# Performance work log

Hardware: AMD Instinct MI355X
Metric: run time of the kernel (lower is better)

Reference implementation:

```python
import jax, jax.numpy as jnp
import numpy as np
import math

S, N, L = 4, 10000, 8
IN, H = 64, 64
D = IN + 2 * H + 1  # rnn input: feats + bidirectional walk enc + degree


def _gru(x, h0, Wih, Whh, bih, bhh, reverse=False):
    """Torch-semantics GRU. x: (B, L, Din), h0: (B, H). Gate order r,z,n."""
    xw = jnp.einsum('bld,gd->blg', x, Wih) + bih  # precompute input proj (B,L,3H)

    def step(h, xw_t):
        gh = h @ Whh.T + bhh
        xr, xz, xn = jnp.split(xw_t, 3, axis=-1)
        hr, hz, hn = jnp.split(gh, 3, axis=-1)
        r = jax.nn.sigmoid(xr + hr)
        z = jax.nn.sigmoid(xz + hz)
        n = jnp.tanh(xn + r * hn)
        h = (1.0 - z) * n + z * h
        return h, h

    hT, ys = jax.lax.scan(step, h0, jnp.swapaxes(xw, 0, 1), reverse=reverse)
    return jnp.swapaxes(ys, 0, 1), hT  # (B,L,H), (B,H)


def setup_inputs() -> dict:
    key = jax.random.key(0)
    ks = jax.random.split(key, 16)
    w = lambda k, shape: (jax.random.normal(k, shape, jnp.float32) * 0.1)
    inp = {
        'h': jax.random.normal(ks[0], (N, IN), jnp.float32),
        'walks': jax.random.randint(ks[1], (S, N, L), 0, N, dtype=jnp.int32),
        'in_degrees': jax.random.randint(ks[2], (N,), 1, 50, dtype=jnp.int32),
        # bidirectional walk GRU (input=2)
        'Wih_f': w(ks[3], (3 * H, 2)), 'Whh_f': w(ks[4], (3 * H, H)),
        'bih_f': w(ks[5], (3 * H,)), 'bhh_f': w(ks[6], (3 * H,)),
        'Wih_b': w(ks[7], (3 * H, 2)), 'Whh_b': w(ks[8], (3 * H, H)),
        'bih_b': w(ks[9], (3 * H,)), 'bhh_b': w(ks[10], (3 * H,)),
        # main GRU (input=D)
        'Wih': w(ks[11], (3 * H, D)), 'Whh': w(ks[12], (3 * H, H)),
        'bih': w(ks[13], (3 * H,)), 'bhh': w(ks[14], (3 * H,)),
    }
    return inp


def reference(h, walks, in_degrees, Wih_f, Whh_f, bih_f, bhh_f,
              Wih_b, Whh_b, bih_b, bhh_b, Wih, Whh, bih, bhh):
    S_, N_, L_ = walks.shape
    # uniqueness: first-occurrence index of each node within its walk
    eq = walks[..., :, None] == walks[..., None, :]          # (S,N,L,L)
    u = jnp.argmax(eq, axis=-1).astype(h.dtype)              # (S,N,L)
    walks = walks[..., ::-1]
    u = u[..., ::-1]
    u = (u / L_) * (2.0 * math.pi)
    uw = jnp.stack([jnp.sin(u), jnp.cos(u)], axis=-1)        # (S,N,L,2)

    hw = h[walks]                                            # gather (S,N,L,IN)
    deg = in_degrees.astype(h.dtype)[walks][..., None]       # (S,N,L,1)
    deg = deg / deg.max()

    B = S_ * N_
    uw2 = uw.reshape(B, L_, 2)
    h0 = jnp.zeros((B, H), h.dtype)
    yf, hf = _gru(uw2, h0, Wih_f, Whh_f, bih_f, bhh_f)
    yb, hb = _gru(uw2, h0, Wih_b, Whh_b, bih_b, bhh_b, reverse=True)
    y_walk = jnp.concatenate([yf, yb], axis=-1).reshape(S_, N_, L_, 2 * H)
    h_walk = 0.5 * (hf + hb)                                 # mean over directions (B,H)

    x = jnp.concatenate([hw, y_walk, deg], axis=-1).reshape(B, L_, D)
    _, hT = _gru(x, h_walk, Wih, Whh, bih, bhh)
    # final hidden has layer dim of size 1; .mean(0) is identity -> (S,N,H)
    out = hT.reshape(S_, N_, H)
    return out
```

## Files before the change

### kernel.cpp

```cpp
#include <hip/hip_runtime.h>
#include <hip/hip_bf16.h>

#define NN   10000
#define SS   4
#define BB   40000
#define LLEN 8
#define DD   193
#define G3   192

typedef __attribute__((ext_vector_type(8))) short bf16x8;
typedef __attribute__((ext_vector_type(4))) short short4v;
typedef __attribute__((ext_vector_type(4))) float f32x4;

#define OFF_DMAX 0
#define OFF_DEGN 1024
#define OFF_A    65536
#define OFF_YF   (8ull*1024*1024)
#define OFF_YB   (49ull*1024*1024)
#define OFF_HFB  (90ull*1024*1024)

__device__ __forceinline__ float sigm(float x){ return 1.0f/(1.0f+__expf(-x)); }
__device__ __forceinline__ float tanh_(float x){
  float e = __expf(-2.0f*fabsf(x));
  float t = (1.0f-e)/(1.0f+e);
  return x>=0.0f ? t : -t;
}
__device__ __forceinline__ short f2b(float f){
  unsigned u = __builtin_bit_cast(unsigned, f);
  u = u + 0x7FFFu + ((u>>16)&1u);
  return (short)(u>>16);
}
__device__ __forceinline__ float b2f(short s){
  unsigned u = ((unsigned)(unsigned short)s)<<16;
  return __builtin_bit_cast(float, u);
}

__global__ void k_zero(int* dmax){
  if (threadIdx.x==0 && blockIdx.x==0) *dmax = 0;
}

__global__ void k_degmax(const int* __restrict__ walks, const int* __restrict__ indeg,
                         int* __restrict__ dmax){
  int i = blockIdx.x*blockDim.x + threadIdx.x;
  int d = 0;
  if (i < SS*NN*LLEN) d = indeg[walks[i]];
  #pragma unroll
  for (int off=32; off>0; off>>=1) d = max(d, __shfl_xor(d, off));
  if ((threadIdx.x&63)==0 && d>0) atomicMax(dmax, d);
}

__global__ void k_degn(const int* __restrict__ indeg, const int* __restrict__ dmax,
                       float* __restrict__ degn){
  int n = blockIdx.x*blockDim.x + threadIdx.x;
  if (n < NN) degn[n] = (float)indeg[n] / (float)(*dmax);
}

__global__ __launch_bounds__(192) void k_A(const float* __restrict__ h,
                                           const float* __restrict__ Wih,
                                           const float* __restrict__ bih,
                                           float* __restrict__ A){
  int g = threadIdx.x;
  float w[64];
  #pragma unroll
  for (int k=0;k<64;++k) w[k] = Wih[g*DD + k];
  float bg = bih[g];
  __shared__ float hs[64];
  int n0 = blockIdx.x*32;
  for (int j=0;j<32;++j){
    int n = n0 + j;
    if (n >= NN) break;
    __syncthreads();
    if (g < 64) hs[g] = h[n*64+g];
    __syncthreads();
    float acc = bg;
    #pragma unroll
    for (int k=0;k<64;++k) acc += w[k]*hs[k];
    A[n*G3 + g] = acc;
  }
}

__global__ __launch_bounds__(256,3) void k_fb(
    const int* __restrict__ walks,
    const float* __restrict__ Wih_f, const float* __restrict__ Whh_f,
    const float* __restrict__ bih_f, const float* __restrict__ bhh_f,
    const float* __restrict__ Wih_b, const float* __restrict__ Whh_b,
    const float* __restrict__ bih_b, const float* __restrict__ bhh_b,
    short* __restrict__ yf_out, short* __restrict__ yb_out,
    short* __restrict__ hfb)
{
  const int dir = blockIdx.y;
  const float* Wih = dir ? Wih_b : Wih_f;
  const float* Whh = dir ? Whh_b : Whh_f;
  const float* bih = dir ? bih_b : bih_f;
  const float* bhh = dir ? bhh_b : bhh_f;
  short* yout = dir ? yb_out : yf_out;

  __shared__ __align__(16) short Wlds[192*64];
  __shared__ __align__(16) short A2[192*8];
  __shared__ __align__(16) short hl[64*64];
  __shared__ __align__(16) float sc[64*8*2];
  __shared__ __align__(16) float bhn[64];

  const int tid = threadIdx.x;
  const int b0  = blockIdx.x*64;

  for (int idx = tid; idx < 192*64; idx += 256){
    int g = idx>>6, k = idx&63;
    Wlds[g*64 + (k ^ ((g&7)<<3))] = f2b(Whh[idx]);
  }
  for (int g = tid; g < 192; g += 256){
    A2[g*8+0] = f2b(Wih[2*g]);
    A2[g*8+1] = f2b(Wih[2*g+1]);
    float bb = bih[g] + (g < 128 ? bhh[g] : 0.0f);
    A2[g*8+2] = f2b(bb);
    A2[g*8+3]=0; A2[g*8+4]=0; A2[g*8+5]=0; A2[g*8+6]=0; A2[g*8+7]=0;
  }
  if (tid < 64) bhn[tid] = bhh[128+tid];
  for (int idx = tid; idx < 512; idx += 256){
    int s = idx>>3, t = idx&7, p = 7-t;
    const int* wr = walks + (long)(b0+s)*LLEN;
    int wp = wr[p]; int u = 7;
    #pragma unroll
    for (int j=7;j>=0;--j) if (wr[j]==wp) u = j;
    float si, ci;
    __sincosf((float)u * 0.7853981633974483f, &si, &ci);
    sc[idx*2] = si; sc[idx*2+1] = ci;
  }
  __syncthreads();

  const int lane = tid & 63;
  const int wv   = tid >> 6;
  const int c    = lane & 15;
  const int a    = lane >> 4;
  const int s    = wv*16 + c;
  const int sg   = b0 + s;

  float hreg[4][4];
  short4v z4 = {0,0,0,0};
  #pragma unroll
  for (int q=0;q<4;++q){
    #pragma unroll
    for (int r=0;r<4;++r) hreg[q][r] = 0.0f;
    int i0 = q*16 + 4*a;
    *(short4v*)&hl[s*64 + (i0 ^ ((s&7)<<3))] = z4;
  }

  for (int ss=0; ss<8; ++ss){
    const int t = dir ? 7-ss : ss;
    asm volatile("s_waitcnt lgkmcnt(0)" ::: "memory");
    bf16x8 bh0 = *(const bf16x8*)&hl[s*64 + ((a*8)      ^ ((s&7)<<3))];
    bf16x8 bh1 = *(const bf16x8*)&hl[s*64 + ((32 + a*8) ^ ((s&7)<<3))];
    bf16x8 b2 = {0,0,0,0,0,0,0,0};
    if (a == 0){
      b2[0] = f2b(sc[(s*8+t)*2]);
      b2[1] = f2b(sc[(s*8+t)*2+1]);
      b2[2] = (short)0x3F80;
    }
    f32x4 acc1[12]; f32x4 acc2[4];
    #pragma unroll
    for (int T=0;T<12;++T){ acc1[T].x=0;acc1[T].y=0;acc1[T].z=0;acc1[T].w=0; }
    #pragma unroll
    for (int T=0;T<4;++T){ acc2[T].x=0;acc2[T].y=0;acc2[T].z=0;acc2[T].w=0; }

    #pragma unroll
    for (int T=0;T<12;++T){
      int g = 16*T + c;
      bf16x8 a0 = *(const bf16x8*)&Wlds[g*64 + ((a*8)      ^ ((g&7)<<3))];
      bf16x8 a1 = *(const bf16x8*)&Wlds[g*64 + ((32 + a*8) ^ ((g&7)<<3))];
      acc1[T] = __builtin_amdgcn_mfma_f32_16x16x32_bf16(a0, bh0, acc1[T], 0,0,0);
      acc1[T] = __builtin_amdgcn_mfma_f32_16x16x32_bf16(a1, bh1, acc1[T], 0,0,0);
      bf16x8 a2 = *(const bf16x8*)&A2[g*8];
      if (T < 8) acc1[T]   = __builtin_amdgcn_mfma_f32_16x16x32_bf16(a2, b2, acc1[T],   0,0,0);
      else       acc2[T-8] = __builtin_amdgcn_mfma_f32_16x16x32_bf16(a2, b2, acc2[T-8], 0,0,0);
    }

    #pragma unroll
    for (int q=0;q<4;++q){
      int i0 = q*16 + 4*a;
      f32x4 bv = *(const f32x4*)&bhn[i0];
      short4v pack;
      #pragma unroll
      for (int r=0;r<4;++r){
        float rr = sigm(acc1[q][r]);
        float zz = sigm(acc1[4+q][r]);
        float hn = acc1[8+q][r] + bv[r];
        float xn = acc2[q][r];
        float nn = tanh_(xn + rr*hn);
        float hv = (1.0f-zz)*nn + zz*hreg[q][r];
        hreg[q][r] = hv;
        pack[r] = f2b(hv);
      }
      *(short4v*)&hl[s*64 + (i0 ^ ((s&7)<<3))] = pack;
      int kb = 4*q + a;
      *(short4v*)(yout + ((long)(t*16+kb)*BB + sg)*4) = pack;
    }
  }

  #pragma unroll
  for (int q=0;q<4;++q){
    int i0 = q*16 + 4*a;
    short4v pk;
    #pragma unroll
    for (int r=0;r<4;++r) pk[r] = f2b(hreg[q][r]);
    *(short4v*)(hfb + ((long)dir*BB + sg)*64 + i0) = pk;
  }
}

__global__ __launch_bounds__(256,1) void k_final(
    const int* __restrict__ walks, const float* __restrict__ degn,
    const float* __restrict__ A,
    const float* __restrict__ W, const float* __restrict__ U,
    const float* __restrict__ bhh,
    const short* __restrict__ yf, const short* __restrict__ yb,
    const short* __restrict__ hfb,
    float* __restrict__ out)
{
  __shared__ __align__(16) short Ulds[192*64];
  __shared__ __align__(16) short Wy[192*128];
  __shared__ __align__(16) short A5[192*8];
  __shared__ __align__(16) short hl[64*64];
  __shared__ __align__(16) int   node[64*8];
  __shared__ __align__(16) float degl[64*8];
  __shared__ __align__(16) float bhn[64];

  const int tid = threadIdx.x;
  const int b0  = blockIdx.x*64;

  for (int idx = tid; idx < 192*64; idx += 256){
    int g = idx>>6, k = idx&63;
    Ulds[g*64 + (k ^ ((g&7)<<3))] = f2b(U[idx]);
  }
  for (int idx = tid; idx < 192*128; idx += 256){
    int g = idx>>7, k2 = idx&127;
    Wy[g*128 + (k2 ^ ((g&7)<<3))] = f2b(W[(long)g*DD + 64 + k2]);
  }
  for (int g = tid; g < 192; g += 256){
    A5[g*8+0] = f2b(W[(long)g*DD + 192]);
    A5[g*8+1] = (g < 128) ? f2b(bhh[g]) : (short)0;
    A5[g*8+2]=0; A5[g*8+3]=0; A5[g*8+4]=0; A5[g*8+5]=0; A5[g*8+6]=0; A5[g*8+7]=0;
  }
  if (tid < 64) bhn[tid] = bhh[128+tid];
  for (int idx = tid; idx < 512; idx += 256){
    int s = idx>>3, t = idx&7;
    int nd = walks[(long)(b0+s)*LLEN + 7-t];
    node[idx] = nd;
    degl[idx] = degn[nd];
  }
  __syncthreads();

  const int lane = tid & 63;
  const int wv   = tid >> 6;
  const int c    = lane & 15;
  const int a    = lane >> 4;
  const int s    = wv*16 + c;
  const int sg   = b0 + s;

  float hreg[4][4];
  #pragma unroll
  for (int q=0;q<4;++q){
    int i0 = q*16 + 4*a;
    short4v hf4 = *(const short4v*)(hfb + (long)sg*64 + i0);
    short4v hb4 = *(const short4v*)(hfb + ((long)BB + sg)*64 + i0);
    short4v pk;
    #pragma unroll
    for (int r=0;r<4;++r){
      float hv = 0.5f*(b2f(hf4[r]) + b2f(hb4[r]));
      hreg[q][r] = hv;
      pk[r] = f2b(hv);
    }
    *(short4v*)&hl[s*64 + (i0 ^ ((s&7)<<3))] = pk;
  }

  auto ldy = [&](const short* Y, int t, int kh, bf16x8& dst){
    int ky0 = kh*32 + a*8;
    int kb  = ky0 >> 2;
    long base = ((long)(t*16 + kb)*BB + sg)*4;
    short4v lo = *(const short4v*)(Y + base);
    short4v hi = *(const short4v*)(Y + base + (long)BB*4);
    dst[0]=lo[0]; dst[1]=lo[1]; dst[2]=lo[2]; dst[3]=lo[3];
    dst[4]=hi[0]; dst[5]=hi[1]; dst[6]=hi[2]; dst[7]=hi[3];
  };

  bf16x8 yfc[2], ybc[2];
  ldy(yf, 0, 0, yfc[0]); ldy(yf, 0, 1, yfc[1]);
  ldy(yb, 0, 0, ybc[0]); ldy(yb, 0, 1, ybc[1]);

  for (int t=0; t<8; ++t){
    bf16x8 yfn[2], ybn[2];
    if (t < 7){
      ldy(yf, t+1, 0, yfn[0]); ldy(yf, t+1, 1, yfn[1]);
      ldy(yb, t+1, 0, ybn[0]); ldy(yb, t+1, 1, ybn[1]);
    }
    int nd = node[s*8 + t];
    f32x4 Ag[12];
    #pragma unroll
    for (int T=0;T<12;++T) Ag[T] = *(const f32x4*)(A + (long)nd*192 + 16*T + 4*a);

    asm volatile("s_waitcnt lgkmcnt(0)" ::: "memory");
    bf16x8 bh0 = *(const bf16x8*)&hl[s*64 + ((a*8)      ^ ((s&7)<<3))];
    bf16x8 bh1 = *(const bf16x8*)&hl[s*64 + ((32 + a*8) ^ ((s&7)<<3))];
    bf16x8 b5 = {0,0,0,0,0,0,0,0};
    if (a == 0){
      b5[0] = f2b(degl[s*8+t]);
      b5[1] = (short)0x3F80;
    }

    f32x4 acc1[12]; f32x4 acc2[4];
    #pragma unroll
    for (int T=0;T<12;++T){ acc1[T].x=0;acc1[T].y=0;acc1[T].z=0;acc1[T].w=0; }
    #pragma unroll
    for (int T=0;T<4;++T){ acc2[T].x=0;acc2[T].y=0;acc2[T].z=0;acc2[T].w=0; }

    #pragma unroll
    for (int T=0;T<12;++T){
      int g = 16*T + c;
      bf16x8 u0 = *(const bf16x8*)&Ulds[g*64 + ((a*8)      ^ ((g&7)<<3))];
      bf16x8 u1 = *(const bf16x8*)&Ulds[g*64 + ((32 + a*8) ^ ((g&7)<<3))];
      acc1[T] = __builtin_amdgcn_mfma_f32_16x16x32_bf16(u0, bh0, acc1[T], 0,0,0);
      acc1[T] = __builtin_amdgcn_mfma_f32_16x16x32_bf16(u1, bh1, acc1[T], 0,0,0);
      bf16x8 w0 = *(const bf16x8*)&Wy[g*128 + ((a*8)       ^ ((g&7)<<3))];
      bf16x8 w1 = *(const bf16x8*)&Wy[g*128 + ((32 + a*8)  ^ ((g&7)<<3))];
      bf16x8 w2 = *(const bf16x8*)&Wy[g*128 + ((64 + a*8)  ^ ((g&7)<<3))];
      bf16x8 w3 = *(const bf16x8*)&Wy[g*128 + ((96 + a*8)  ^ ((g&7)<<3))];
      bf16x8 a5 = *(const bf16x8*)&A5[g*8];
      if (T < 8){
        acc1[T] = __builtin_amdgcn_mfma_f32_16x16x32_bf16(w0, yfc[0], acc1[T], 0,0,0);
        acc1[T] = __builtin_amdgcn_mfma_f32_16x16x32_bf16(w1, yfc[1], acc1[T], 0,0,0);
        acc1[T] = __builtin_amdgcn_mfma_f32_16x16x32_bf16(w2, ybc[0], acc1[T], 0,0,0);
        acc1[T] = __builtin_amdgcn_mfma_f32_16x16x32_bf16(w3, ybc[1], acc1[T], 0,0,0);
        acc1[T] = __builtin_amdgcn_mfma_f32_16x16x32_bf16(a5, b5,     acc1[T], 0,0,0);
      } else {
        acc2[T-8] = __builtin_amdgcn_mfma_f32_16x16x32_bf16(w0, yfc[0], acc2[T-8], 0,0,0);
        acc2[T-8] = __builtin_amdgcn_mfma_f32_16x16x32_bf16(w1, yfc[1], acc2[T-8], 0,0,0);
        acc2[T-8] = __builtin_amdgcn_mfma_f32_16x16x32_bf16(w2, ybc[0], acc2[T-8], 0,0,0);
        acc2[T-8] = __builtin_amdgcn_mfma_f32_16x16x32_bf16(w3, ybc[1], acc2[T-8], 0,0,0);
        acc2[T-8] = __builtin_amdgcn_mfma_f32_16x16x32_bf16(a5, b5,     acc2[T-8], 0,0,0);
      }
    }

    #pragma unroll
    for (int q=0;q<4;++q){
      int i0 = q*16 + 4*a;
      f32x4 bv = *(const f32x4*)&bhn[i0];
      short4v pack;
      #pragma unroll
      for (int r=0;r<4;++r){
        float rr = sigm(acc1[q][r]   + Ag[q][r]);
        float zz = sigm(acc1[4+q][r] + Ag[4+q][r]);
        float hn = acc1[8+q][r] + bv[r];
        float xn = acc2[q][r]   + Ag[8+q][r];
        float nn = tanh_(xn + rr*hn);
        float hv = (1.0f-zz)*nn + zz*hreg[q][r];
        hreg[q][r] = hv;
        pack[r] = f2b(hv);
      }
      *(short4v*)&hl[s*64 + (i0 ^ ((s&7)<<3))] = pack;
    }

    if (t < 7){
      yfc[0]=yfn[0]; yfc[1]=yfn[1];
      ybc[0]=ybn[0]; ybc[1]=ybn[1];
    }
  }

  #pragma unroll
  for (int q=0;q<4;++q){
    int i0 = q*16 + 4*a;
    f32x4 o;
    #pragma unroll
    for (int r=0;r<4;++r) o[r] = hreg[q][r];
    *(f32x4*)(out + (long)sg*64 + i0) = o;
  }
}

extern "C" void kernel_launch(void* const* d_in, const int* in_sizes, int n_in,
                              void* d_out, int out_size, void* d_ws, size_t ws_size,
                              hipStream_t stream) {
  const float* h     = (const float*)d_in[0];
  const int*   walks = (const int*)d_in[1];
  const int*   indeg = (const int*)d_in[2];
  const float* Wf    = (const float*)d_in[3];
  const float* Uf    = (const float*)d_in[4];
  const float* bif   = (const float*)d_in[5];
  const float* bhf   = (const float*)d_in[6];
  const float* Wb    = (const float*)d_in[7];
  const float* Ub    = (const float*)d_in[8];
  const float* bib   = (const float*)d_in[9];
  const float* bhb   = (const float*)d_in[10];
  const float* W     = (const float*)d_in[11];
  const float* U     = (const float*)d_in[12];
  const float* bi    = (const float*)d_in[13];
  const float* bh    = (const float*)d_in[14];
  float* out = (float*)d_out;

  char* ws = (char*)d_ws;
  int*   dmax = (int*)(ws + OFF_DMAX);
  float* degn = (float*)(ws + OFF_DEGN);
  float* A    = (float*)(ws + OFF_A);
  short* yfw  = (short*)(ws + OFF_YF);
  short* ybw  = (short*)(ws + OFF_YB);
  short* hfb  = (short*)(ws + OFF_HFB);

  k_zero<<<1, 64, 0, stream>>>(dmax);
  k_degmax<<<(SS*NN*LLEN + 255)/256, 256, 0, stream>>>(walks, indeg, dmax);
  k_degn<<<(NN + 255)/256, 256, 0, stream>>>(indeg, dmax, degn);
  k_A<<<(NN + 31)/32, 192, 0, stream>>>(h, W, bi, A);
  k_fb<<<dim3(BB/64, 2), 256, 0, stream>>>(walks,
                                           Wf, Uf, bif, bhf,
                                           Wb, Ub, bib, bhb,
                                           yfw, ybw, hfb);
  k_final<<<BB/64, 256, 0, stream>>>(walks, degn, A, W, U, bh,
                                     yfw, ybw, hfb, out);
}
```

Before: 383.5 us.

## Prepack weights into MFMA fragment blob and drop per-block LDS weight staging

A new prep kernel converts all GRU weights and bias vectors once into bf16, laid out in MFMA A-fragment order in global memory. k_fb and k_final then read these fragments straight from global/L2 instead of having every block convert and stage the full weight matrices in LDS. Blocks shrink to 128 threads, each wave now handles two 16-sequence groups so every weight fragment load feeds two MFMAs, and LDS use drops so more blocks fit per CU. The cost is repeated weight fragment loads from cache on every timestep. The prefetch of y inputs for the next step in k_final is also removed.

```diff
diff --git a/kernel.cpp b/kernel.cpp
--- a/kernel.cpp
+++ b/kernel.cpp
@@ -14,10 +14,14 @@
 
 #define OFF_DMAX 0
 #define OFF_DEGN 1024
-#define OFF_A    65536
+#define OFF_FRAG 65536
+#define OFF_A    262144
 #define OFF_YF   (8ull*1024*1024)
 #define OFF_YB   (49ull*1024*1024)
 #define OFF_HFB  (90ull*1024*1024)
+
+#define FB_FRAG(dir,T,ch)  (((dir)*12 + (T))*3 + (ch))
+#define FIN_FRAG(T,ch)     (72 + (T)*7 + (ch))
 
 __device__ __forceinline__ float sigm(float x){ return 1.0f/(1.0f+__expf(-x)); }
 __device__ __forceinline__ float tanh_(float x){
@@ -53,6 +57,58 @@
                        float* __restrict__ degn){
   int n = blockIdx.x*blockDim.x + threadIdx.x;
   if (n < NN) degn[n] = (float)indeg[n] / (float)(*dmax);
+}
+
+__global__ __launch_bounds__(64) void k_prep(
+    const float* __restrict__ Wih_f, const float* __restrict__ Whh_f,
+    const float* __restrict__ bih_f, const float* __restrict__ bhh_f,
+    const float* __restrict__ Wih_b, const float* __restrict__ Whh_b,
+    const float* __restrict__ bih_b, const float* __restrict__ bhh_b,
+    const float* __restrict__ W, const float* __restrict__ U,
+    const float* __restrict__ bhh,
+    short* __restrict__ blob)
+{
+  int f = blockIdx.x;
+  int lane = threadIdx.x;
+  int c = lane & 15, a = lane >> 4;
+  float v[8];
+  if (f < 72){
+    int dir = f / 36, rem = f % 36, T = rem / 3, ch = rem % 3;
+    int g = 16*T + c;
+    const float* Whh = dir ? Whh_b : Whh_f;
+    const float* Wih = dir ? Wih_b : Wih_f;
+    const float* bih = dir ? bih_b : bih_f;
+    const float* bhd = dir ? bhh_b : bhh_f;
+    if (ch < 2){
+      #pragma unroll
+      for (int j=0;j<8;++j) v[j] = Whh[g*64 + ch*32 + a*8 + j];
+    } else {
+      #pragma unroll
+      for (int j=0;j<8;++j){
+        int k = a*8 + j;
+        v[j] = (k==0) ? Wih[2*g] : (k==1) ? Wih[2*g+1]
+             : (k==2) ? (bih[g] + (g<128 ? bhd[g] : 0.0f)) : 0.0f;
+      }
+    }
+  } else {
+    int f2 = f - 72, T = f2 / 7, ch = f2 % 7;
+    int g = 16*T + c;
+    if (ch < 2){
+      #pragma unroll
+      for (int j=0;j<8;++j) v[j] = U[g*64 + ch*32 + a*8 + j];
+    } else if (ch < 6){
+      #pragma unroll
+      for (int j=0;j<8;++j) v[j] = W[(long)g*DD + 64 + (ch-2)*32 + a*8 + j];
+    } else {
+      #pragma unroll
+      for (int j=0;j<8;++j){
+        int k = a*8 + j;
+        v[j] = (k==0) ? W[(long)g*DD + 192] : (k==1) ? (g<128 ? bhh[g] : 0.0f) : 0.0f;
+      }
+    }
+  }
+  #pragma unroll
+  for (int j=0;j<8;++j) blob[(long)f*512 + lane*8 + j] = f2b(v[j]);
 }
 
 __global__ __launch_bounds__(192) void k_A(const float* __restrict__ h,
@@ -79,24 +135,16 @@
   }
 }
 
-__global__ __launch_bounds__(256,3) void k_fb(
-    const int* __restrict__ walks,
-    const float* __restrict__ Wih_f, const float* __restrict__ Whh_f,
-    const float* __restrict__ bih_f, const float* __restrict__ bhh_f,
-    const float* __restrict__ Wih_b, const float* __restrict__ Whh_b,
-    const float* __restrict__ bih_b, const float* __restrict__ bhh_b,
+__global__ __launch_bounds__(128, 2) void k_fb(
+    const int* __restrict__ walks, const short* __restrict__ blob,
+    const float* __restrict__ bhh_f, const float* __restrict__ bhh_b,
     short* __restrict__ yf_out, short* __restrict__ yb_out,
     short* __restrict__ hfb)
 {
   const int dir = blockIdx.y;
-  const float* Wih = dir ? Wih_b : Wih_f;
-  const float* Whh = dir ? Whh_b : Whh_f;
-  const float* bih = dir ? bih_b : bih_f;
   const float* bhh = dir ? bhh_b : bhh_f;
   short* yout = dir ? yb_out : yf_out;
 
-  __shared__ __align__(16) short Wlds[192*64];
-  __shared__ __align__(16) short A2[192*8];
   __shared__ __align__(16) short hl[64*64];
   __shared__ __align__(16) float sc[64*8*2];
   __shared__ __align__(16) float bhn[64];
@@ -104,19 +152,8 @@
   const int tid = threadIdx.x;
   const int b0  = blockIdx.x*64;
 
-  for (int idx = tid; idx < 192*64; idx += 256){
-    int g = idx>>6, k = idx&63;
-    Wlds[g*64 + (k ^ ((g&7)<<3))] = f2b(Whh[idx]);
-  }
-  for (int g = tid; g < 192; g += 256){
-    A2[g*8+0] = f2b(Wih[2*g]);
-    A2[g*8+1] = f2b(Wih[2*g+1]);
-    float bb = bih[g] + (g < 128 ? bhh[g] : 0.0f);
-    A2[g*8+2] = f2b(bb);
-    A2[g*8+3]=0; A2[g*8+4]=0; A2[g*8+5]=0; A2[g*8+6]=0; A2[g*8+7]=0;
-  }
   if (tid < 64) bhn[tid] = bhh[128+tid];
-  for (int idx = tid; idx < 512; idx += 256){
+  for (int idx = tid; idx < 512; idx += 128){
     int s = idx>>3, t = idx&7, p = 7-t;
     const int* wr = walks + (long)(b0+s)*LLEN;
     int wp = wr[p]; int u = 7;
@@ -126,98 +163,115 @@
     __sincosf((float)u * 0.7853981633974483f, &si, &ci);
     sc[idx*2] = si; sc[idx*2+1] = ci;
   }
-  __syncthreads();
 
   const int lane = tid & 63;
   const int wv   = tid >> 6;
   const int c    = lane & 15;
   const int a    = lane >> 4;
-  const int s    = wv*16 + c;
-  const int sg   = b0 + s;
-
-  float hreg[4][4];
+  const int s0   = wv*32 + c;
+  const int s1   = wv*32 + 16 + c;
+
+  float hreg[2][4][4];
   short4v z4 = {0,0,0,0};
   #pragma unroll
-  for (int q=0;q<4;++q){
-    #pragma unroll
-    for (int r=0;r<4;++r) hreg[q][r] = 0.0f;
-    int i0 = q*16 + 4*a;
-    *(short4v*)&hl[s*64 + (i0 ^ ((s&7)<<3))] = z4;
-  }
+  for (int sb=0;sb<2;++sb){
+    int s = sb ? s1 : s0;
+    #pragma unroll
+    for (int q=0;q<4;++q){
+      #pragma unroll
+      for (int r=0;r<4;++r) hreg[sb][q][r] = 0.0f;
+      int i0 = q*16 + 4*a;
+      *(short4v*)&hl[s*64 + (i0 ^ ((s&7)<<3))] = z4;
+    }
+  }
+  __syncthreads();
+
+  const bf16x8* FB = (const bf16x8*)blob;
 
   for (int ss=0; ss<8; ++ss){
     const int t = dir ? 7-ss : ss;
     asm volatile("s_waitcnt lgkmcnt(0)" ::: "memory");
-    bf16x8 bh0 = *(const bf16x8*)&hl[s*64 + ((a*8)      ^ ((s&7)<<3))];
-    bf16x8 bh1 = *(const bf16x8*)&hl[s*64 + ((32 + a*8) ^ ((s&7)<<3))];
-    bf16x8 b2 = {0,0,0,0,0,0,0,0};
-    if (a == 0){
-      b2[0] = f2b(sc[(s*8+t)*2]);
-      b2[1] = f2b(sc[(s*8+t)*2+1]);
-      b2[2] = (short)0x3F80;
-    }
-    f32x4 acc1[12]; f32x4 acc2[4];
-    #pragma unroll
-    for (int T=0;T<12;++T){ acc1[T].x=0;acc1[T].y=0;acc1[T].z=0;acc1[T].w=0; }
-    #pragma unroll
-    for (int T=0;T<4;++T){ acc2[T].x=0;acc2[T].y=0;acc2[T].z=0;acc2[T].w=0; }
-
-    #pragma unroll
-    for (int T=0;T<12;++T){
-      int g = 16*T + c;
-      bf16x8 a0 = *(const bf16x8*)&Wlds[g*64 + ((a*8)      ^ ((g&7)<<3))];
-      bf16x8 a1 = *(const bf16x8*)&Wlds[g*64 + ((32 + a*8) ^ ((g&7)<<3))];
-      acc1[T] = __builtin_amdgcn_mfma_f32_16x16x32_bf16(a0, bh0, acc1[T], 0,0,0);
-      acc1[T] = __builtin_amdgcn_mfma_f32_16x16x32_bf16(a1, bh1, acc1[T], 0,0,0);
-      bf16x8 a2 = *(const bf16x8*)&A2[g*8];
-      if (T < 8) acc1[T]   = __builtin_amdgcn_mfma_f32_16x16x32_bf16(a2, b2, acc1[T],   0,0,0);
-      else       acc2[T-8] = __builtin_amdgcn_mfma_f32_16x16x32_bf16(a2, b2, acc2[T-8], 0,0,0);
-    }
-
+    bf16x8 bh0[2], bh1[2], b2[2];
+    #pragma unroll
+    for (int sb=0;sb<2;++sb){
+      int s = sb ? s1 : s0;
+      bh0[sb] = *(const bf16x8*)&hl[s*64 + ((a*8)      ^ ((s&7)<<3))];
+      bh1[sb] = *(const bf16x8*)&hl[s*64 + ((32 + a*8) ^ ((s&7)<<3))];
+      float si = sc[(s*8+t)*2], ci = sc[(s*8+t)*2+1];
+      bf16x8 bb = {0,0,0,0,0,0,0,0};
+      if (a == 0){ bb[0] = f2b(si); bb[1] = f2b(ci); bb[2] = (short)0x3F80; }
+      b2[sb] = bb;
+    }
+
+    #pragma unroll
+    for (int q=0;q<4;++q){
+      f32x4 ar[2], az[2], an1[2], an2[2];
+      #pragma unroll
+      for (int sb=0;sb<2;++sb){
+        ar[sb].x=0;ar[sb].y=0;ar[sb].z=0;ar[sb].w=0;
+        az[sb]=ar[sb]; an1[sb]=ar[sb]; an2[sb]=ar[sb];
+      }
+      #pragma unroll
+      for (int ch=0;ch<3;++ch){
+        bf16x8 fr = FB[(long)FB_FRAG(dir,   q,ch)*64 + lane];
+        bf16x8 fz = FB[(long)FB_FRAG(dir, 4+q,ch)*64 + lane];
+        bf16x8 fn = FB[(long)FB_FRAG(dir, 8+q,ch)*64 + lane];
+        #pragma unroll
+        for (int sb=0;sb<2;++sb){
+          bf16x8 bb = (ch==0) ? bh0[sb] : (ch==1) ? bh1[sb] : b2[sb];
+          ar[sb] = __builtin_amdgcn_mfma_f32_16x16x32_bf16(fr, bb, ar[sb], 0,0,0);
+          az[sb] = __builtin_amdgcn_mfma_f32_16x16x32_bf16(fz, bb, az[sb], 0,0,0);
+          if (ch < 2) an1[sb] = __builtin_amdgcn_mfma_f32_16x16x32_bf16(fn, bb, an1[sb], 0,0,0);
+          else        an2[sb] = __builtin_amdgcn_mfma_f32_16x16x32_bf16(fn, bb, an2[sb], 0,0,0);
+        }
+      }
+      f32x4 bv = *(const f32x4*)&bhn[q*16 + 4*a];
+      #pragma unroll
+      for (int sb=0;sb<2;++sb){
+        int s = sb ? s1 : s0;
+        int sg = b0 + s;
+        short4v pack;
+        #pragma unroll
+        for (int r=0;r<4;++r){
+          float rr = sigm(ar[sb][r]);
+          float zz = sigm(az[sb][r]);
+          float hn_ = an1[sb][r] + bv[r];
+          float xn  = an2[sb][r];
+          float nn = tanh_(xn + rr*hn_);
+          float hv = (1.0f-zz)*nn + zz*hreg[sb][q][r];
+          hreg[sb][q][r] = hv;
+          pack[r] = f2b(hv);
+        }
+        int i0 = q*16 + 4*a;
+        *(short4v*)&hl[s*64 + (i0 ^ ((s&7)<<3))] = pack;
+        *(short4v*)(yout + ((long)(t*16 + 4*q + a)*BB + sg)*4) = pack;
+      }
+    }
+  }
+
+  #pragma unroll
+  for (int sb=0;sb<2;++sb){
+    int s = sb ? s1 : s0;
+    int sg = b0 + s;
     #pragma unroll
     for (int q=0;q<4;++q){
       int i0 = q*16 + 4*a;
-      f32x4 bv = *(const f32x4*)&bhn[i0];
-      short4v pack;
-      #pragma unroll
-      for (int r=0;r<4;++r){
-        float rr = sigm(acc1[q][r]);
-        float zz = sigm(acc1[4+q][r]);
-        float hn = acc1[8+q][r] + bv[r];
-        float xn = acc2[q][r];
-        float nn = tanh_(xn + rr*hn);
-        float hv = (1.0f-zz)*nn + zz*hreg[q][r];
-        hreg[q][r] = hv;
-        pack[r] = f2b(hv);
-      }
-      *(short4v*)&hl[s*64 + (i0 ^ ((s&7)<<3))] = pack;
-      int kb = 4*q + a;
-      *(short4v*)(yout + ((long)(t*16+kb)*BB + sg)*4) = pack;
-    }
-  }
-
-  #pragma unroll
-  for (int q=0;q<4;++q){
-    int i0 = q*16 + 4*a;
-    short4v pk;
-    #pragma unroll
-    for (int r=0;r<4;++r) pk[r] = f2b(hreg[q][r]);
-    *(short4v*)(hfb + ((long)dir*BB + sg)*64 + i0) = pk;
-  }
-}
-
-__global__ __launch_bounds__(256,1) void k_final(
+      short4v pk;
+      #pragma unroll
+      for (int r=0;r<4;++r) pk[r] = f2b(hreg[sb][q][r]);
+      *(short4v*)(hfb + ((long)dir*BB + sg)*64 + i0) = pk;
+    }
+  }
+}
+
+__global__ __launch_bounds__(128, 2) void k_final(
     const int* __restrict__ walks, const float* __restrict__ degn,
-    const float* __restrict__ A,
-    const float* __restrict__ W, const float* __restrict__ U,
+    const float* __restrict__ A, const short* __restrict__ blob,
     const float* __restrict__ bhh,
     const short* __restrict__ yf, const short* __restrict__ yb,
     const short* __restrict__ hfb,
     float* __restrict__ out)
 {
-  __shared__ __align__(16) short Ulds[192*64];
-  __shared__ __align__(16) short Wy[192*128];
-  __shared__ __align__(16) short A5[192*8];
   __shared__ __align__(16) short hl[64*64];
   __shared__ __align__(16) int   node[64*8];
   __shared__ __align__(16) float degl[64*8];
@@ -226,54 +280,47 @@
   const int tid = threadIdx.x;
   const int b0  = blockIdx.x*64;
 
-  for (int idx = tid; idx < 192*64; idx += 256){
-    int g = idx>>6, k = idx&63;
-    Ulds[g*64 + (k ^ ((g&7)<<3))] = f2b(U[idx]);
-  }
-  for (int idx = tid; idx < 192*128; idx += 256){
-    int g = idx>>7, k2 = idx&127;
-    Wy[g*128 + (k2 ^ ((g&7)<<3))] = f2b(W[(long)g*DD + 64 + k2]);
-  }
-  for (int g = tid; g < 192; g += 256){
-    A5[g*8+0] = f2b(W[(long)g*DD + 192]);
-    A5[g*8+1] = (g < 128) ? f2b(bhh[g]) : (short)0;
-    A5[g*8+2]=0; A5[g*8+3]=0; A5[g*8+4]=0; A5[g*8+5]=0; A5[g*8+6]=0; A5[g*8+7]=0;
-  }
   if (tid < 64) bhn[tid] = bhh[128+tid];
-  for (int idx = tid; idx < 512; idx += 256){
+  for (int idx = tid; idx < 512; idx += 128){
     int s = idx>>3, t = idx&7;
     int nd = walks[(long)(b0+s)*LLEN + 7-t];
     node[idx] = nd;
     degl[idx] = degn[nd];
   }
-  __syncthreads();
 
   const int lane = tid & 63;
   const int wv   = tid >> 6;
   const int c    = lane & 15;
   const int a    = lane >> 4;
-  const int s    = wv*16 + c;
-  const int sg   = b0 + s;
-
-  float hreg[4][4];
-  #pragma unroll
-  for (int q=0;q<4;++q){
-    int i0 = q*16 + 4*a;
-    short4v hf4 = *(const short4v*)(hfb + (long)sg*64 + i0);
-    short4v hb4 = *(const short4v*)(hfb + ((long)BB + sg)*64 + i0);
-    short4v pk;
-    #pragma unroll
-    for (int r=0;r<4;++r){
-      float hv = 0.5f*(b2f(hf4[r]) + b2f(hb4[r]));
-      hreg[q][r] = hv;
-      pk[r] = f2b(hv);
-    }
-    *(short4v*)&hl[s*64 + (i0 ^ ((s&7)<<3))] = pk;
-  }
-
-  auto ldy = [&](const short* Y, int t, int kh, bf16x8& dst){
-    int ky0 = kh*32 + a*8;
-    int kb  = ky0 >> 2;
+  const int s0   = wv*32 + c;
+  const int s1   = wv*32 + 16 + c;
+
+  float hreg[2][4][4];
+  #pragma unroll
+  for (int sb=0;sb<2;++sb){
+    int s = sb ? s1 : s0;
+    int sg = b0 + s;
+    #pragma unroll
+    for (int q=0;q<4;++q){
+      int i0 = q*16 + 4*a;
+      short4v hf4 = *(const short4v*)(hfb + (long)sg*64 + i0);
+      short4v hb4 = *(const short4v*)(hfb + ((long)BB + sg)*64 + i0);
+      short4v pk;
+      #pragma unroll
+      for (int r=0;r<4;++r){
+        float hv = 0.5f*(b2f(hf4[r]) + b2f(hb4[r]));
+        hreg[sb][q][r] = hv;
+        pk[r] = f2b(hv);
+      }
+      *(short4v*)&hl[s*64 + (i0 ^ ((s&7)<<3))] = pk;
+    }
+  }
+  __syncthreads();
+
+  const bf16x8* FB = (const bf16x8*)blob;
+
+  auto ldy = [&](const short* Y, int t, int kh, int sg, bf16x8& dst){
+    int kb  = kh*8 + a*2;
     long base = ((long)(t*16 + kb)*BB + sg)*4;
     short4v lo = *(const short4v*)(Y + base);
     short4v hi = *(const short4v*)(Y + base + (long)BB*4);
@@ -281,95 +328,86 @@
     dst[4]=hi[0]; dst[5]=hi[1]; dst[6]=hi[2]; dst[7]=hi[3];
   };
 
-  bf16x8 yfc[2], ybc[2];
-  ldy(yf, 0, 0, yfc[0]); ldy(yf, 0, 1, yfc[1]);
-  ldy(yb, 0, 0, ybc[0]); ldy(yb, 0, 1, ybc[1]);
-
   for (int t=0; t<8; ++t){
-    bf16x8 yfn[2], ybn[2];
-    if (t < 7){
-      ldy(yf, t+1, 0, yfn[0]); ldy(yf, t+1, 1, yfn[1]);
-      ldy(yb, t+1, 0, ybn[0]); ldy(yb, t+1, 1, ybn[1]);
-    }
-    int nd = node[s*8 + t];
-    f32x4 Ag[12];
-    #pragma unroll
-    for (int T=0;T<12;++T) Ag[T] = *(const f32x4*)(A + (long)nd*192 + 16*T + 4*a);
-
     asm volatile("s_waitcnt lgkmcnt(0)" ::: "memory");
-    bf16x8 bh0 = *(const bf16x8*)&hl[s*64 + ((a*8)      ^ ((s&7)<<3))];
-    bf16x8 bh1 = *(const bf16x8*)&hl[s*64 + ((32 + a*8) ^ ((s&7)<<3))];
-    bf16x8 b5 = {0,0,0,0,0,0,0,0};
-    if (a == 0){
-      b5[0] = f2b(degl[s*8+t]);
-      b5[1] = (short)0x3F80;
-    }
-
-    f32x4 acc1[12]; f32x4 acc2[4];
-    #pragma unroll
-    for (int T=0;T<12;++T){ acc1[T].x=0;acc1[T].y=0;acc1[T].z=0;acc1[T].w=0; }
-    #pragma unroll
-    for (int T=0;T<4;++T){ acc2[T].x=0;acc2[T].y=0;acc2[T].z=0;acc2[T].w=0; }
-
-    #pragma unroll
-    for (int T=0;T<12;++T){
-      int g = 16*T + c;
-      bf16x8 u0 = *(const bf16x8*)&Ulds[g*64 + ((a*8)      ^ ((g&7)<<3))];
-      bf16x8 u1 = *(const bf16x8*)&Ulds[g*64 + ((32 + a*8) ^ ((g&7)<<3))];
-      acc1[T] = __builtin_amdgcn_mfma_f32_16x16x32_bf16(u0, bh0, acc1[T], 0,0,0);
-      acc1[T] = __builtin_amdgcn_mfma_f32_16x16x32_bf16(u1, bh1, acc1[T], 0,0,0);
-      bf16x8 w0 = *(const bf16x8*)&Wy[g*128 + ((a*8)       ^ ((g&7)<<3))];
-      bf16x8 w1 = *(const bf16x8*)&Wy[g*128 + ((32 + a*8)  ^ ((g&7)<<3))];
-      bf16x8 w2 = *(const bf16x8*)&Wy[g*128 + ((64 + a*8)  ^ ((g&7)<<3))];
-      bf16x8 w3 = *(const bf16x8*)&Wy[g*128 + ((96 + a*8)  ^ ((g&7)<<3))];
-      bf16x8 a5 = *(const bf16x8*)&A5[g*8];
-      if (T < 8){
-        acc1[T] = __builtin_amdgcn_mfma_f32_16x16x32_bf16(w0, yfc[0], acc1[T], 0,0,0);
-        acc1[T] = __builtin_amdgcn_mfma_f32_16x16x32_bf16(w1, yfc[1], acc1[T], 0,0,0);
-        acc1[T] = __builtin_amdgcn_mfma_f32_16x16x32_bf16(w2, ybc[0], acc1[T], 0,0,0);
-        acc1[T] = __builtin_amdgcn_mfma_f32_16x16x32_bf16(w3, ybc[1], acc1[T], 0,0,0);
-        acc1[T] = __builtin_amdgcn_mfma_f32_16x16x32_bf16(a5, b5,     acc1[T], 0,0,0);
-      } else {
-        acc2[T-8] = __builtin_amdgcn_mfma_f32_16x16x32_bf16(w0, yfc[0], acc2[T-8], 0,0,0);
-        acc2[T-8] = __builtin_amdgcn_mfma_f32_16x16x32_bf16(w1, yfc[1], acc2[T-8], 0,0,0);
-        acc2[T-8] = __builtin_amdgcn_mfma_f32_16x16x32_bf16(w2, ybc[0], acc2[T-8], 0,0,0);
-        acc2[T-8] = __builtin_amdgcn_mfma_f32_16x16x32_bf16(w3, ybc[1], acc2[T-8], 0,0,0);
-        acc2[T-8] = __builtin_amdgcn_mfma_f32_16x16x32_bf16(a5, b5,     acc2[T-8], 0,0,0);
-      }
-    }
-
+    bf16x8 bh0[2], bh1[2], b5[2], yfc[2][2], ybc[2][2];
+    int nd_[2];
+    #pragma unroll
+    for (int sb=0;sb<2;++sb){
+      int s = sb ? s1 : s0;
+      int sg = b0 + s;
+      bh0[sb] = *(const bf16x8*)&hl[s*64 + ((a*8)      ^ ((s&7)<<3))];
+      bh1[sb] = *(const bf16x8*)&hl[s*64 + ((32 + a*8) ^ ((s&7)<<3))];
+      bf16x8 bb = {0,0,0,0,0,0,0,0};
+      if (a == 0){ bb[0] = f2b(degl[s*8+t]); bb[1] = (short)0x3F80; }
+      b5[sb] = bb;
+      ldy(yf, t, 0, sg, yfc[sb][0]); ldy(yf, t, 1, sg, yfc[sb][1]);
+      ldy(yb, t, 0, sg, ybc[sb][0]); ldy(yb, t, 1, sg, ybc[sb][1]);
+      nd_[sb] = node[s*8 + t];
+    }
+
+    #pragma unroll
+    for (int q=0;q<4;++q){
+      f32x4 ar[2], az[2], an1[2], an2[2];
+      #pragma unroll
+      for (int sb=0;sb<2;++sb){
+        ar[sb].x=0;ar[sb].y=0;ar[sb].z=0;ar[sb].w=0;
+        az[sb]=ar[sb]; an1[sb]=ar[sb]; an2[sb]=ar[sb];
+      }
+      #pragma unroll
+      for (int ch=0;ch<7;++ch){
+        bf16x8 fr = FB[(long)FIN_FRAG(   q,ch)*64 + lane];
+        bf16x8 fz = FB[(long)FIN_FRAG( 4+q,ch)*64 + lane];
+        bf16x8 fn = FB[(long)FIN_FRAG( 8+q,ch)*64 + lane];
+        #pragma unroll
+        for (int sb=0;sb<2;++sb){
+          bf16x8 bb = (ch==0) ? bh0[sb] : (ch==1) ? bh1[sb]
+                    : (ch==2) ? yfc[sb][0] : (ch==3) ? yfc[sb][1]
+                    : (ch==4) ? ybc[sb][0] : (ch==5) ? ybc[sb][1] : b5[sb];
+          ar[sb] = __builtin_amdgcn_mfma_f32_16x16x32_bf16(fr, bb, ar[sb], 0,0,0);
+          az[sb] = __builtin_amdgcn_mfma_f32_16x16x32_bf16(fz, bb, az[sb], 0,0,0);
+          if (ch < 2) an1[sb] = __builtin_amdgcn_mfma_f32_16x16x32_bf16(fn, bb, an1[sb], 0,0,0);
+          else        an2[sb] = __builtin_amdgcn_mfma_f32_16x16x32_bf16(fn, bb, an2[sb], 0,0,0);
+        }
+      }
+      f32x4 bv = *(const f32x4*)&bhn[q*16 + 4*a];
+      #pragma unroll
+      for (int sb=0;sb<2;++sb){
+        int s = sb ? s1 : s0;
+        const float* Ab = A + (long)nd_[sb]*G3 + q*16 + 4*a;
+        f32x4 Agr = *(const f32x4*)(Ab);
+        f32x4 Agz = *(const f32x4*)(Ab + 64);
+        f32x4 Agn = *(const f32x4*)(Ab + 128);
+        short4v pack;
+        #pragma unroll
+        for (int r=0;r<4;++r){
+          float rr = sigm(ar[sb][r]  + Agr[r]);
+          float zz = sigm(az[sb][r]  + Agz[r]);
+          float hn_ = an1[sb][r] + bv[r];
+          float xn  = an2[sb][r] + Agn[r];
+          float nn = tanh_(xn + rr*hn_);
+          float hv = (1.0f-zz)*nn + zz*hreg[sb][q][r];
+          hreg[sb][q][r] = hv;
+          pack[r] = f2b(hv);
+        }
+        int i0 = q*16 + 4*a;
+        *(short4v*)&hl[s*64 + (i0 ^ ((s&7)<<3))] = pack;
+      }
+    }
+  }
+
+  #pragma unroll
+  for (int sb=0;sb<2;++sb){
+    int s = sb ? s1 : s0;
+    int sg = b0 + s;
     #pragma unroll
     for (int q=0;q<4;++q){
       int i0 = q*16 + 4*a;
-      f32x4 bv = *(const f32x4*)&bhn[i0];
-      short4v pack;
-      #pragma unroll
-      for (int r=0;r<4;++r){
-        float rr = sigm(acc1[q][r]   + Ag[q][r]);
-        float zz = sigm(acc1[4+q][r] + Ag[4+q][r]);
-        float hn = acc1[8+q][r] + bv[r];
-        float xn = acc2[q][r]   + Ag[8+q][r];
-        float nn = tanh_(xn + rr*hn);
-        float hv = (1.0f-zz)*nn + zz*hreg[q][r];
-        hreg[q][r] = hv;
-        pack[r] = f2b(hv);
-      }
-      *(short4v*)&hl[s*64 + (i0 ^ ((s&7)<<3))] = pack;
-    }
-
-    if (t < 7){
-      yfc[0]=yfn[0]; yfc[1]=yfn[1];
-      ybc[0]=ybn[0]; ybc[1]=ybn[1];
-    }
-  }
-
-  #pragma unroll
-  for (int q=0;q<4;++q){
-    int i0 = q*16 + 4*a;
-    f32x4 o;
-    #pragma unroll
-    for (int r=0;r<4;++r) o[r] = hreg[q][r];
-    *(f32x4*)(out + (long)sg*64 + i0) = o;
+      f32x4 o;
+      #pragma unroll
+      for (int r=0;r<4;++r) o[r] = hreg[sb][q][r];
+      *(f32x4*)(out + (long)sg*64 + i0) = o;
+    }
   }
 }
 
@@ -396,6 +434,7 @@
   char* ws = (char*)d_ws;
   int*   dmax = (int*)(ws + OFF_DMAX);
   float* degn = (float*)(ws + OFF_DEGN);
+  short* blob = (short*)(ws + OFF_FRAG);
   float* A    = (float*)(ws + OFF_A);
   short* yfw  = (short*)(ws + OFF_YF);
   short* ybw  = (short*)(ws + OFF_YB);
@@ -404,11 +443,8 @@
   k_zero<<<1, 64, 0, stream>>>(dmax);
   k_degmax<<<(SS*NN*LLEN + 255)/256, 256, 0, stream>>>(walks, indeg, dmax);
   k_degn<<<(NN + 255)/256, 256, 0, stream>>>(indeg, dmax, degn);
+  k_prep<<<156, 64, 0, stream>>>(Wf, Uf, bif, bhf, Wb, Ub, bib, bhb, W, U, bh, blob);
   k_A<<<(NN + 31)/32, 192, 0, stream>>>(h, W, bi, A);
-  k_fb<<<dim3(BB/64, 2), 256, 0, stream>>>(walks,
-                                           Wf, Uf, bif, bhf,
-                                           Wb, Ub, bib, bhb,
-                                           yfw, ybw, hfb);
-  k_final<<<BB/64, 256, 0, stream>>>(walks, degn, A, W, U, bh,
-                                     yfw, ybw, hfb, out);
-}
+  k_fb<<<dim3(BB/64, 2), 128, 0, stream>>>(walks, blob, bhf, bhb, yfw, ybw, hfb);
+  k_final<<<BB/64, 128, 0, stream>>>(walks, degn, A, blob, bh, yfw, ybw, hfb, out);
+}
```

Measured after the change: 478.1 us. 1.25x slower.
